# Performance work log

Hardware: AMD Instinct MI355X
Metric: run time of the kernel (lower is better)

## Reference

```python
import jax, jax.numpy as jnp
import numpy as np

P = 5        # window_size
HEADS = 8
DH = 32      # dim_head
SCALE = DH ** -0.5


def setup_inputs() -> dict:
    key = jax.random.key(0)
    ks = jax.random.split(key, 5)
    b, c, h = 32, 256, 4000
    inner = HEADS * DH  # 256
    x = jax.random.normal(ks[0], (b, c, h), dtype=jnp.float32)
    W_qkv = jax.random.normal(ks[1], (c, inner * 3), dtype=jnp.float32) * (c ** -0.5)
    W_out = jax.random.normal(ks[2], (inner, c), dtype=jnp.float32) * (inner ** -0.5)
    b_out = jax.random.normal(ks[3], (c,), dtype=jnp.float32) * 0.02
    pos_embedding = jax.random.normal(ks[4], (2 * P - 1, 2 * P - 1), dtype=jnp.float32) * 0.02
    return {"x": x, "W_qkv": W_qkv, "W_out": W_out, "b_out": b_out, "pos_embedding": pos_embedding}


def _local_attn(x, W_qkv, W_out, b_out, pos_embedding):
    b, c, h = x.shape
    n = h // P
    # relative-position bias, faithful to torch indexing: rel_index[:,0]=(p-1-a), rel_index[:,1]=(p-a), shape (p,1)
    a = jnp.arange(P)
    bias = pos_embedding[(P - 1 - a)[:, None], (P - a)[:, None]]  # (p, 1)
    mask = jnp.zeros((P, P), x.dtype) + bias                      # (p, p)
    # 'b c (n p) -> (b n) p c'
    xw = x.reshape(b, c, n, P).transpose(0, 2, 3, 1).reshape(b * n, P, c)
    qkv = xw @ W_qkv  # (B, p, 3*inner)
    q, k, v = jnp.split(qkv, 3, axis=-1)
    split_heads = lambda t: t.reshape(b * n, P, HEADS, DH).transpose(0, 2, 1, 3)  # (B, h, p, d)
    q, k, v = split_heads(q), split_heads(k), split_heads(v)
    dots = jnp.einsum('bhid,bhjd->bhij', q, k) * SCALE + mask
    attn = jax.nn.softmax(dots, axis=-1)
    out = jnp.einsum('bhij,bhjd->bhid', attn, v)            # (B, h, p, d)
    out = out.transpose(0, 2, 1, 3).reshape(b * n, P, HEADS * DH)
    out = out @ W_out + b_out                                # (B, p, c_out)
    # '(b n) p c -> b c (n p)'
    out = out.reshape(b, n, P, -1).transpose(0, 3, 1, 2).reshape(b, -1, n * P)
    return out, attn


def reference(x, W_qkv, W_out, b_out, pos_embedding):
    return _local_attn(x, W_qkv, W_out, b_out, pos_embedding)
```

## Files before the change

### kernel.cpp

```cpp
#include <hip/hip_runtime.h>
#include <hip/hip_bf16.h>

typedef __attribute__((ext_vector_type(8))) short short8;
typedef __attribute__((ext_vector_type(4))) float f32x4;

namespace {
constexpr int kC = 256;
constexpr int kH = 4000;
constexpr int kNW = 800;
constexpr int kP = 5;
constexpr float kScale = 0.17677669529663687f;
constexpr int kTotalWin = 25600;

constexpr int WPB = 6;
constexpr int ROWS = WPB * kP;
constexpr int MT = 2;
constexpr int NTHR = 512;

constexpr int WQKV_PACKED = 3 * 16 * 8 * 64 * 8;
constexpr int WOUT_PACKED = 16 * 8 * 64 * 8;

constexpr int RKOFF = 15360;
constexpr int RVT = 30720;
constexpr int SM_TOTAL = 47104;
}

__device__ inline float b2f(short s) {
  union { unsigned u; float f; } v;
  v.u = ((unsigned)(unsigned short)s) << 16;
  return v.f;
}
__device__ inline unsigned short f2bs(float f) {
  __hip_bfloat16 h = __float2bfloat16(f);
  return *reinterpret_cast<unsigned short*>(&h);
}

__global__ void prep_weights(const float* __restrict__ Wqkv,
                             const float* __restrict__ Wout,
                             __hip_bfloat16* __restrict__ wq_p,
                             __hip_bfloat16* __restrict__ wo_p) {
  int idx = blockIdx.x * 256 + threadIdx.x;
  if (idx < WQKV_PACKED) {
    int i = idx & 7;
    int l = (idx >> 3) & 63;
    int kt = (idx >> 9) & 7;
    int nt = (idx >> 12) & 15;
    int part = idx >> 16;
    int k = kt * 32 + (l >> 4) * 8 + i;
    int col = part * 256 + nt * 16 + (l & 15);
    wq_p[idx] = __float2bfloat16(Wqkv[k * 768 + col]);
  }
  if (idx < WOUT_PACKED) {
    int i = idx & 7;
    int l = (idx >> 3) & 63;
    int kt = (idx >> 9) & 7;
    int nt = (idx >> 12) & 15;
    int k = kt * 32 + (l >> 4) * 8 + i;
    int col = nt * 16 + (l & 15);
    wo_p[idx] = __float2bfloat16(Wout[k * 256 + col]);
  }
}

__global__ __launch_bounds__(NTHR, 3) void local_attn_kernel(
    const float* __restrict__ x, const short* __restrict__ wq_p,
    const short* __restrict__ wo_p, const float* __restrict__ b_out,
    float* __restrict__ g_out, float* __restrict__ g_attn) {
  __shared__ __align__(16) char smem[SM_TOTAL];

  const int tid = threadIdx.x;
  const int lane = tid & 63;
  const int wid = tid >> 6;

  const int widx0 = blockIdx.x * WPB;
  const int nwin = min(WPB, kTotalWin - widx0);
  const int nrows = nwin * kP;

  for (int i = tid; i < (kC / 2) * ROWS; i += NTHR) {
    int cp = i / ROWS, hh = i % ROWS;
    if (hh < nrows) {
      int gw = widx0 + hh / kP;
      int b = gw / kNW;
      int hl = (gw - b * kNW) * kP + hh % kP;
      const float* p = x + ((size_t)b * kC + 2 * cp) * kH + hl;
      unsigned u = (unsigned)f2bs(p[0]) | ((unsigned)f2bs(p[kH]) << 16);
      *(unsigned*)(smem + hh * 512 + ((cp * 4) ^ ((hh & 7) << 4))) = u;
    }
  }
  if (tid < 256) {
    int h = tid >> 5, d = tid & 31;
    int phys = 3 ^ ((d >> 1) & 3);
    *(unsigned*)(smem + RVT + h * 2048 + d * 64 + phys * 16 + 12) = 0u;
  }
  __syncthreads();

  for (int pi = 0; pi < 2; ++pi) {
    const int part = pi + 1;
    f32x4 acc[MT][2];
#pragma unroll
    for (int m = 0; m < MT; ++m)
#pragma unroll
      for (int n = 0; n < 2; ++n) acc[m][n] = (f32x4){0.f, 0.f, 0.f, 0.f};
#pragma unroll
    for (int kt = 0; kt < 8; ++kt) {
      short8 a[MT];
#pragma unroll
      for (int m = 0; m < MT; ++m) {
        int row = m * 16 + (lane & 15);
        int kb = kt * 64 + ((lane >> 4) << 4);
        a[m] = *(const short8*)(smem + row * 512 + (kb ^ ((row & 7) << 4)));
      }
      short8 b[2];
#pragma unroll
      for (int n = 0; n < 2; ++n) {
        int nt = wid * 2 + n;
        b[n] = *(const short8*)(wq_p +
                                ((((part * 16 + nt) * 8 + kt) * 64 + lane) * 8));
      }
#pragma unroll
      for (int m = 0; m < MT; ++m)
#pragma unroll
        for (int n = 0; n < 2; ++n)
          acc[m][n] = __builtin_amdgcn_mfma_f32_16x16x32_bf16(a[m], b[n],
                                                              acc[m][n], 0, 0, 0);
    }
    if (part == 1) {
#pragma unroll
      for (int m = 0; m < MT; ++m)
#pragma unroll
        for (int n = 0; n < 2; ++n)
#pragma unroll
          for (int r = 0; r < 4; ++r) {
            int row = m * 16 + ((lane >> 4) << 2) + r;
            if (row < ROWS) {
              int col = wid * 32 + n * 16 + (lane & 15);
              *(__hip_bfloat16*)(smem + RKOFF + row * 512 +
                                 ((col * 2) ^ ((row & 7) << 4))) =
                  __float2bfloat16(acc[m][n][r]);
            }
          }
    } else {
#pragma unroll
      for (int m = 0; m < MT; ++m)
#pragma unroll
        for (int n = 0; n < 2; ++n)
#pragma unroll
          for (int r = 0; r < 4; ++r) {
            int ks = m * 16 + ((lane >> 4) << 2) + r;
            if (ks < ROWS) {
              int d = n * 16 + (lane & 15);
              int lb = ks * 2;
              int phys = (lb >> 4) ^ ((d >> 1) & 3);
              *(__hip_bfloat16*)(smem + RVT + wid * 2048 + d * 64 + phys * 16 +
                                 (lb & 15)) = __float2bfloat16(acc[m][n][r]);
            }
          }
    }
  }
  {
    f32x4 accq[MT][2];
#pragma unroll
    for (int m = 0; m < MT; ++m)
#pragma unroll
      for (int n = 0; n < 2; ++n) accq[m][n] = (f32x4){0.f, 0.f, 0.f, 0.f};
#pragma unroll
    for (int kt = 0; kt < 8; ++kt) {
      short8 a[MT];
#pragma unroll
      for (int m = 0; m < MT; ++m) {
        int row = m * 16 + (lane & 15);
        int kb = kt * 64 + ((lane >> 4) << 4);
        a[m] = *(const short8*)(smem + row * 512 + (kb ^ ((row & 7) << 4)));
      }
      short8 b[2];
#pragma unroll
      for (int n = 0; n < 2; ++n) {
        int nt = wid * 2 + n;
        b[n] = *(const short8*)(wq_p + (((nt * 8 + kt) * 64 + lane) * 8));
      }
#pragma unroll
      for (int m = 0; m < MT; ++m)
#pragma unroll
        for (int n = 0; n < 2; ++n)
          accq[m][n] = __builtin_amdgcn_mfma_f32_16x16x32_bf16(a[m], b[n],
                                                               accq[m][n], 0, 0, 0);
    }
    __syncthreads();
#pragma unroll
    for (int m = 0; m < MT; ++m)
#pragma unroll
      for (int n = 0; n < 2; ++n)
#pragma unroll
        for (int r = 0; r < 4; ++r) {
          int row = m * 16 + ((lane >> 4) << 2) + r;
          if (row < ROWS) {
            int col = wid * 32 + n * 16 + (lane & 15);
            *(__hip_bfloat16*)(smem + row * 512 + ((col * 2) ^ ((row & 7) << 4))) =
                __float2bfloat16(accq[m][n][r]);
          }
        }
  }
  __syncthreads();

  f32x4 sacc[2][2];
  {
    short8 qa[2], kb2[2];
#pragma unroll
    for (int mt = 0; mt < 2; ++mt) {
      int row = mt * 16 + (lane & 15);
      qa[mt] = *(const short8*)(smem + row * 512 +
                                ((wid * 64 + ((lane >> 4) << 4)) ^ ((row & 7) << 4)));
    }
#pragma unroll
    for (int nt = 0; nt < 2; ++nt) {
      int row = nt * 16 + (lane & 15);
      kb2[nt] = *(const short8*)(smem + RKOFF + row * 512 +
                                 ((wid * 64 + ((lane >> 4) << 4)) ^ ((row & 7) << 4)));
    }
#pragma unroll
    for (int mt = 0; mt < 2; ++mt)
#pragma unroll
      for (int nt = 0; nt < 2; ++nt)
        sacc[mt][nt] = __builtin_amdgcn_mfma_f32_16x16x32_bf16(
            qa[mt], kb2[nt], (f32x4){0.f, 0.f, 0.f, 0.f}, 0, 0, 0);
  }
  __syncthreads();

#pragma unroll
  for (int mt = 0; mt < 2; ++mt)
#pragma unroll
    for (int nt = 0; nt < 2; ++nt)
#pragma unroll
      for (int r = 0; r < 4; ++r) {
        int qrow = mt * 16 + ((lane >> 4) << 2) + r;
        int krow = nt * 16 + (lane & 15);
        int qw = qrow / 5, kw = krow / 5;
        if (qrow < ROWS && krow < ROWS && qw == kw) {
          int jj = (krow - kw * 5) * 4;
          int phys = (((jj >> 4) ^ ((qrow >> 1) & 3)) << 4) | (jj & 15);
          *(float*)(smem + RKOFF + wid * 1920 + qrow * 64 + phys) =
              sacc[mt][nt][r] * kScale;
        }
      }
  __syncthreads();

  if (tid < 240) {
    int q = tid % 30, h = tid / 30;
    int w = q / 5, i = q - w * 5;
    if (w < nwin) {
      char* base = smem + RKOFF + h * 1920 + q * 64;
      int csw = (q >> 1) & 3;
      float p[5], mx = -1e30f;
#pragma unroll
      for (int j = 0; j < 5; ++j) {
        int jj = j * 4;
        p[j] = *(const float*)(base + ((((jj >> 4) ^ csw) << 4) | (jj & 15)));
        mx = fmaxf(mx, p[j]);
      }
      float sum = 0.f;
#pragma unroll
      for (int j = 0; j < 5; ++j) {
        p[j] = __expf(p[j] - mx);
        sum += p[j];
      }
      float inv = 1.f / sum;
      float* ap = g_attn + (size_t)(widx0 + w) * 200 + h * 25 + i * 5;
#pragma unroll
      for (int j = 0; j < 5; ++j) {
        p[j] *= inv;
        ap[j] = p[j];
      }
      short8 z = (short8){0, 0, 0, 0, 0, 0, 0, 0};
#pragma unroll
      for (int c = 0; c < 4; ++c) *(short8*)(base + c * 16) = z;
#pragma unroll
      for (int j = 0; j < 5; ++j) {
        int lb = (w * 5 + j) * 2;
        *(unsigned short*)(base + ((((lb >> 4) ^ csw) << 4) | (lb & 15))) =
            f2bs(p[j]);
      }
    }
  }
  __syncthreads();

  {
    short8 va[2], pb[2];
#pragma unroll
    for (int mt = 0; mt < 2; ++mt) {
      int d = mt * 16 + (lane & 15);
      int phys = ((lane >> 4) ^ ((d >> 1) & 3)) << 4;
      va[mt] = *(const short8*)(smem + RVT + wid * 2048 + d * 64 + phys);
    }
#pragma unroll
    for (int nt = 0; nt < 2; ++nt) {
      int q = nt * 16 + (lane & 15);
      int phys = ((lane >> 4) ^ ((q >> 1) & 3)) << 4;
      pb[nt] = *(const short8*)(smem + RKOFF + wid * 1920 + q * 64 + phys);
    }
#pragma unroll
    for (int mt = 0; mt < 2; ++mt)
#pragma unroll
      for (int nt = 0; nt < 2; ++nt) {
        f32x4 o = __builtin_amdgcn_mfma_f32_16x16x32_bf16(
            va[mt], pb[nt], (f32x4){0.f, 0.f, 0.f, 0.f}, 0, 0, 0);
#pragma unroll
        for (int r = 0; r < 4; ++r) {
          int d = mt * 16 + ((lane >> 4) << 2) + r;
          int q = nt * 16 + (lane & 15);
          if (q < ROWS) {
            int cb = wid * 64 + d * 2;
            *(__hip_bfloat16*)(smem + q * 512 + (cb ^ ((q & 7) << 4))) =
                __float2bfloat16(o[r]);
          }
        }
      }
  }
  __syncthreads();

  f32x4 acc2[MT][2];
#pragma unroll
  for (int m = 0; m < MT; ++m)
#pragma unroll
    for (int n = 0; n < 2; ++n) acc2[m][n] = (f32x4){0.f, 0.f, 0.f, 0.f};
#pragma unroll
  for (int kt = 0; kt < 8; ++kt) {
    short8 a[MT];
#pragma unroll
    for (int m = 0; m < MT; ++m) {
      int row = m * 16 + (lane & 15);
      int kb = kt * 64 + ((lane >> 4) << 4);
      a[m] = *(const short8*)(smem + row * 512 + (kb ^ ((row & 7) << 4)));
    }
    short8 b[2];
#pragma unroll
    for (int n = 0; n < 2; ++n) {
      int nt = wid * 2 + n;
      b[n] = *(const short8*)(wo_p + (((nt * 8 + kt) * 64 + lane) * 8));
    }
#pragma unroll
    for (int m = 0; m < MT; ++m)
#pragma unroll
      for (int n = 0; n < 2; ++n)
        acc2[m][n] = __builtin_amdgcn_mfma_f32_16x16x32_bf16(a[m], b[n],
                                                             acc2[m][n], 0, 0, 0);
  }
  float* outS = (float*)(smem + RKOFF);
#pragma unroll
  for (int n = 0; n < 2; ++n) {
    int col = wid * 32 + n * 16 + (lane & 15);
    float bias = b_out[col];
#pragma unroll
    for (int m = 0; m < MT; ++m)
#pragma unroll
      for (int r = 0; r < 4; ++r) {
        int row = m * 16 + ((lane >> 4) << 2) + r;
        if (row < ROWS) outS[col * ROWS + row] = acc2[m][n][r] + bias;
      }
  }
  __syncthreads();

  for (int i = tid; i < kC * ROWS; i += NTHR) {
    int c = i / ROWS, hh = i % ROWS;
    if (hh < nrows) {
      int gw = widx0 + hh / kP;
      int b = gw / kNW;
      int hl = (gw - b * kNW) * kP + hh % kP;
      g_out[((size_t)b * kC + c) * kH + hl] = outS[c * ROWS + hh];
    }
  }
}

extern "C" void kernel_launch(void* const* d_in, const int* in_sizes, int n_in,
                              void* d_out, int out_size, void* d_ws,
                              size_t ws_size, hipStream_t stream) {
  const float* x = (const float*)d_in[0];
  const float* Wqkv = (const float*)d_in[1];
  const float* Wout = (const float*)d_in[2];
  const float* bout = (const float*)d_in[3];

  short* wq_p = (short*)d_ws;
  short* wo_p = wq_p + WQKV_PACKED;

  prep_weights<<<WQKV_PACKED / 256, 256, 0, stream>>>(
      Wqkv, Wout, (__hip_bfloat16*)wq_p, (__hip_bfloat16*)wo_p);

  float* g_out = (float*)d_out;
  float* g_attn = g_out + (size_t)32 * kC * kH;

  int nblocks = (kTotalWin + WPB - 1) / WPB;
  local_attn_kernel<<<nblocks, NTHR, 0, stream>>>(x, wq_p, wo_p, bout, g_out,
                                                  g_attn);
}
```

Before: 191.5 us.

## Fuse scores, softmax, and PV into register-resident per-wave attention path

Computes S^T = K·Q^T with MFMA, then rearranges score fragments across lanes with shuffles so each lane holds the B-operand layout for the P·V MFMA. Softmax is evaluated in registers with a window mask and cross-lane sum reductions, which drops the LDS round-trips for scores and probabilities and several block-wide barriers. It also zero-fills the unused tail rows of the tile so out-of-range rows feed zeros. The max subtraction in softmax is removed, which relies on the scores being small enough not to overflow expf.

After: 194.1 us. Within noise of the previous version (+1.4%).

```diff
diff --git a/kernel.cpp b/kernel.cpp
--- a/kernel.cpp
+++ b/kernel.cpp
@@ -25,11 +25,6 @@
 constexpr int SM_TOTAL = 47104;
 }
 
-__device__ inline float b2f(short s) {
-  union { unsigned u; float f; } v;
-  v.u = ((unsigned)(unsigned short)s) << 16;
-  return v.f;
-}
 __device__ inline unsigned short f2bs(float f) {
   __hip_bfloat16 h = __float2bfloat16(f);
   return *reinterpret_cast<unsigned short*>(&h);
@@ -86,6 +81,8 @@
       *(unsigned*)(smem + hh * 512 + ((cp * 4) ^ ((hh & 7) << 4))) = u;
     }
   }
+  for (int i = tid; i < (ROWS - nrows) * 128; i += NTHR)
+    *(unsigned*)(smem + (nrows + i / 128) * 512 + (i % 128) * 4) = 0u;
   if (tid < 256) {
     int h = tid >> 5, d = tid & 31;
     int phys = 3 ^ ((d >> 1) & 3);
@@ -201,118 +198,91 @@
   }
   __syncthreads();
 
-  f32x4 sacc[2][2];
   {
-    short8 qa[2], kb2[2];
-#pragma unroll
-    for (int mt = 0; mt < 2; ++mt) {
-      int row = mt * 16 + (lane & 15);
-      qa[mt] = *(const short8*)(smem + row * 512 +
-                                ((wid * 64 + ((lane >> 4) << 4)) ^ ((row & 7) << 4)));
-    }
-#pragma unroll
-    for (int nt = 0; nt < 2; ++nt) {
-      int row = nt * 16 + (lane & 15);
-      kb2[nt] = *(const short8*)(smem + RKOFF + row * 512 +
-                                 ((wid * 64 + ((lane >> 4) << 4)) ^ ((row & 7) << 4)));
-    }
-#pragma unroll
-    for (int mt = 0; mt < 2; ++mt)
-#pragma unroll
-      for (int nt = 0; nt < 2; ++nt)
-        sacc[mt][nt] = __builtin_amdgcn_mfma_f32_16x16x32_bf16(
-            qa[mt], kb2[nt], (f32x4){0.f, 0.f, 0.f, 0.f}, 0, 0, 0);
-  }
-  __syncthreads();
-
-#pragma unroll
-  for (int mt = 0; mt < 2; ++mt)
-#pragma unroll
-    for (int nt = 0; nt < 2; ++nt)
+    short8 kfa[2], qfb[2], va[2];
+#pragma unroll
+    for (int t = 0; t < 2; ++t) {
+      int row = t * 16 + (lane & 15);
+      int cb = (wid * 64 + ((lane >> 4) << 4)) ^ ((row & 7) << 4);
+      kfa[t] = *(const short8*)(smem + RKOFF + row * 512 + cb);
+      qfb[t] = *(const short8*)(smem + row * 512 + cb);
+      va[t] = *(const short8*)(smem + RVT + wid * 2048 + row * 64 +
+                               (((lane >> 4) ^ ((row >> 1) & 3)) << 4));
+    }
+    f32x4 sacc[2][2];
+#pragma unroll
+    for (int mk = 0; mk < 2; ++mk)
+#pragma unroll
+      for (int nq = 0; nq < 2; ++nq) {
+        sacc[mk][nq] = __builtin_amdgcn_mfma_f32_16x16x32_bf16(
+            kfa[mk], qfb[nq], (f32x4){0.f, 0.f, 0.f, 0.f}, 0, 0, 0);
+#pragma unroll
+        for (int r = 0; r < 4; ++r) sacc[mk][nq][r] *= kScale;
+      }
+
+    const int g = lane >> 4;
+    const int alo = ((g & 1) << 1) * 16 + (lane & 15);
+    const int ahi = alo + 16;
+    const bool ghi = g >= 2;
+
+#pragma unroll
+    for (int nq = 0; nq < 2; ++nq) {
+      const int q_abs = nq * 16 + (lane & 15);
+      float s8[8];
 #pragma unroll
       for (int r = 0; r < 4; ++r) {
-        int qrow = mt * 16 + ((lane >> 4) << 2) + r;
-        int krow = nt * 16 + (lane & 15);
-        int qw = qrow / 5, kw = krow / 5;
-        if (qrow < ROWS && krow < ROWS && qw == kw) {
-          int jj = (krow - kw * 5) * 4;
-          int phys = (((jj >> 4) ^ ((qrow >> 1) & 3)) << 4) | (jj & 15);
-          *(float*)(smem + RKOFF + wid * 1920 + qrow * 64 + phys) =
-              sacc[mt][nt][r] * kScale;
+        float v0l = __shfl(sacc[0][nq][r], alo);
+        float v1l = __shfl(sacc[1][nq][r], alo);
+        float v0h = __shfl(sacc[0][nq][r], ahi);
+        float v1h = __shfl(sacc[1][nq][r], ahi);
+        s8[r] = ghi ? v1l : v0l;
+        s8[4 + r] = ghi ? v1h : v0h;
+      }
+      const int w = q_abs / 5;
+      const int lo = w * 5;
+      float p8[8], psum = 0.f;
+#pragma unroll
+      for (int i = 0; i < 8; ++i) {
+        int kk = g * 8 + i;
+        bool in = (q_abs < ROWS) && (kk >= lo) && (kk < lo + 5);
+        float e = in ? __expf(s8[i]) : 0.f;
+        p8[i] = e;
+        psum += e;
+      }
+      psum += __shfl_xor(psum, 16);
+      psum += __shfl_xor(psum, 32);
+      float inv = psum > 0.f ? 1.f / psum : 0.f;
+      short8 pb;
+#pragma unroll
+      for (int i = 0; i < 8; ++i) {
+        p8[i] *= inv;
+        pb[i] = (short)f2bs(p8[i]);
+      }
+      if (q_abs < nrows) {
+        int iq = q_abs - lo;
+        float* ap =
+            g_attn + (size_t)(widx0 + w) * 200 + wid * 25 + iq * 5 - lo;
+#pragma unroll
+        for (int i = 0; i < 8; ++i) {
+          int kk = g * 8 + i;
+          if (kk >= lo && kk < lo + 5) ap[kk] = p8[i];
         }
       }
-  __syncthreads();
-
-  if (tid < 240) {
-    int q = tid % 30, h = tid / 30;
-    int w = q / 5, i = q - w * 5;
-    if (w < nwin) {
-      char* base = smem + RKOFF + h * 1920 + q * 64;
-      int csw = (q >> 1) & 3;
-      float p[5], mx = -1e30f;
-#pragma unroll
-      for (int j = 0; j < 5; ++j) {
-        int jj = j * 4;
-        p[j] = *(const float*)(base + ((((jj >> 4) ^ csw) << 4) | (jj & 15)));
-        mx = fmaxf(mx, p[j]);
-      }
-      float sum = 0.f;
-#pragma unroll
-      for (int j = 0; j < 5; ++j) {
-        p[j] = __expf(p[j] - mx);
-        sum += p[j];
-      }
-      float inv = 1.f / sum;
-      float* ap = g_attn + (size_t)(widx0 + w) * 200 + h * 25 + i * 5;
-#pragma unroll
-      for (int j = 0; j < 5; ++j) {
-        p[j] *= inv;
-        ap[j] = p[j];
-      }
-      short8 z = (short8){0, 0, 0, 0, 0, 0, 0, 0};
-#pragma unroll
-      for (int c = 0; c < 4; ++c) *(short8*)(base + c * 16) = z;
-#pragma unroll
-      for (int j = 0; j < 5; ++j) {
-        int lb = (w * 5 + j) * 2;
-        *(unsigned short*)(base + ((((lb >> 4) ^ csw) << 4) | (lb & 15))) =
-            f2bs(p[j]);
-      }
-    }
-  }
-  __syncthreads();
-
-  {
-    short8 va[2], pb[2];
-#pragma unroll
-    for (int mt = 0; mt < 2; ++mt) {
-      int d = mt * 16 + (lane & 15);
-      int phys = ((lane >> 4) ^ ((d >> 1) & 3)) << 4;
-      va[mt] = *(const short8*)(smem + RVT + wid * 2048 + d * 64 + phys);
-    }
-#pragma unroll
-    for (int nt = 0; nt < 2; ++nt) {
-      int q = nt * 16 + (lane & 15);
-      int phys = ((lane >> 4) ^ ((q >> 1) & 3)) << 4;
-      pb[nt] = *(const short8*)(smem + RKOFF + wid * 1920 + q * 64 + phys);
-    }
-#pragma unroll
-    for (int mt = 0; mt < 2; ++mt)
-#pragma unroll
-      for (int nt = 0; nt < 2; ++nt) {
+#pragma unroll
+      for (int mt = 0; mt < 2; ++mt) {
         f32x4 o = __builtin_amdgcn_mfma_f32_16x16x32_bf16(
-            va[mt], pb[nt], (f32x4){0.f, 0.f, 0.f, 0.f}, 0, 0, 0);
-#pragma unroll
-        for (int r = 0; r < 4; ++r) {
-          int d = mt * 16 + ((lane >> 4) << 2) + r;
-          int q = nt * 16 + (lane & 15);
-          if (q < ROWS) {
-            int cb = wid * 64 + d * 2;
-            *(__hip_bfloat16*)(smem + q * 512 + (cb ^ ((q & 7) << 4))) =
+            va[mt], pb, (f32x4){0.f, 0.f, 0.f, 0.f}, 0, 0, 0);
+        if (q_abs < ROWS) {
+          int qsw = (q_abs & 7) << 4;
+#pragma unroll
+          for (int r = 0; r < 4; ++r) {
+            int d = mt * 16 + g * 4 + r;
+            *(__hip_bfloat16*)(smem + q_abs * 512 + ((wid * 64 + d * 2) ^ qsw)) =
                 __float2bfloat16(o[r]);
           }
         }
       }
+    }
   }
   __syncthreads();
 
```
